# Kernel optimization log

Measured on AMD Instinct MI355X. Metric: run time of the kernel, lower is better.

Reference implementation:

```python
import jax, jax.numpy as jnp
import numpy as np

# dims
B, V, IMG = 16, 2, 224
G, PATCH, SG = 7, 14, 16
D, NH, L = 768, 12, 12
DH = D // NH            # 64
P = DH // 4             # rope frequencies per axis (2D axial RoPE)
N = G * G               # 49 glimpse tokens
S = SG * SG             # 256 scene tokens
GSIZE = G * PATCH       # 98 px glimpse


def _ln(x, w, b):
    m = x.mean(-1, keepdims=True)
    v = ((x - m) ** 2).mean(-1, keepdims=True)
    return (x - m) * jax.lax.rsqrt(v + 1e-6) * w + b


def _rope(pos, periods):
    # pos [B,N,2] -> cos,sin [B,N,2P]  (x freqs then y freqs)
    ang = (pos[..., :, None] / periods).reshape(pos.shape[0], pos.shape[1], -1)
    return jnp.cos(ang), jnp.sin(ang)


def _apply_rope(x, cos, sin):
    # x [B,H,N,DH]; cos/sin [B,N,DH//2]
    c = cos[:, None, :, :]
    s = sin[:, None, :, :]
    xr = x.reshape(x.shape[0], x.shape[1], x.shape[2], DH // 2, 2)
    x1, x2 = xr[..., 0], xr[..., 1]
    return jnp.stack([x1 * c - x2 * s, x1 * s + x2 * c], -1).reshape(x.shape)


def _heads(x):
    return x.reshape(x.shape[0], x.shape[1], NH, DH).transpose(0, 2, 1, 3)


def _merge(x):
    return x.transpose(0, 2, 1, 3).reshape(x.shape[0], x.shape[2], D)


def _attn(q, k, v):
    a = jax.nn.softmax(jnp.einsum('bhqd,bhkd->bhqk', q, k) / jnp.sqrt(jnp.float32(DH)), axis=-1)
    return jnp.einsum('bhqk,bhkd->bhqd', a, v)


def _cross(xq, xkv, qw, qb, kvw, kvb, ow, ob, rq, rkv):
    q = _heads(xq @ qw.T + qb)
    kv = xkv @ kvw.T + kvb
    k, v = _heads(kv[..., :D]), _heads(kv[..., D:])
    q = _apply_rope(q, *rq)
    k = _apply_rope(k, *rkv)
    return _merge(_attn(q, k, v)) @ ow.T + ob


def _bilinear(img, py, px):
    # img [C,H,W], py/px [GSIZE] pixel coords -> [C,GSIZE,GSIZE]
    Hh, Ww = img.shape[1], img.shape[2]
    y0 = jnp.clip(jnp.floor(py), 0, Hh - 2).astype(jnp.int32)
    x0 = jnp.clip(jnp.floor(px), 0, Ww - 2).astype(jnp.int32)
    wy = jnp.clip(py - y0, 0.0, 1.0)[None, :, None]
    wx = jnp.clip(px - x0, 0.0, 1.0)[None, None, :]
    g0, g1 = img[:, y0, :], img[:, y0 + 1, :]
    v00, v01 = g0[:, :, x0], g0[:, :, x0 + 1]
    v10, v11 = g1[:, :, x0], g1[:, :, x0 + 1]
    return (v00 * (1 - wy) + v10 * wy) * (1 - wx) + (v01 * (1 - wy) + v11 * wy) * wx


def _extract(images, c, s):
    # crop a [-1,1]-normalized glimpse of half-width `scale` at `center`
    lin = jnp.linspace(-1.0, 1.0, GSIZE)
    gy = c[:, 1:2] + s[:, None] * lin
    gx = c[:, 0:1] + s[:, None] * lin
    py = (gy + 1.0) * 0.5 * (images.shape[2] - 1)
    px = (gx + 1.0) * 0.5 * (images.shape[3] - 1)
    return jax.vmap(_bilinear)(images, py, px)


def _forward(images, centers, scales, patch_w, patch_b, scene_tokens,
             ln1_w, ln1_b, ln2_w, ln2_b, qkv_w, qkv_b, attn_out_w, attn_out_b,
             mlp_w1, mlp_b1, mlp_w2, mlp_b2,
             read_q_w, read_q_b, read_kv_w, read_kv_b, read_out_w, read_out_b, read_gate,
             write_q_w, write_q_b, write_kv_w, write_kv_b, write_out_w, write_out_b, write_gate):
    periods = 100.0 ** (jnp.arange(P, dtype=jnp.float32) / P)
    lin_s = jnp.linspace(-1.0, 1.0, SG)
    ys, xs = jnp.meshgrid(lin_s, lin_s, indexing='ij')
    scene_pos = jnp.broadcast_to(jnp.stack([xs.ravel(), ys.ravel()], -1), (B, S, 2))
    scene_rope = _rope(scene_pos, periods)
    lin_g = jnp.linspace(-1.0, 1.0, G)
    yg, xg = jnp.meshgrid(lin_g, lin_g, indexing='ij')
    goffs = jnp.stack([xg.ravel(), yg.ravel()], -1)  # [N,2]

    scene = jnp.broadcast_to(scene_tokens, (B, S, D))
    for vp in range(V):
        glimpse = _extract(images, centers[vp], scales[vp])  # [B,3,98,98]
        t = jax.lax.conv_general_dilated(glimpse, patch_w, (PATCH, PATCH), 'VALID',
                                         dimension_numbers=('NCHW', 'OIHW', 'NCHW'))
        local = t.reshape(B, D, N).transpose(0, 2, 1) + patch_b  # [B,49,D]
        lpos = centers[vp][:, None, :] + scales[vp][:, None, None] * goffs
        lrope = _rope(lpos, periods)
        for i in range(L):
            local = local + read_gate[i] * _cross(local, scene,
                read_q_w[i], read_q_b[i], read_kv_w[i], read_kv_b[i],
                read_out_w[i], read_out_b[i], lrope, scene_rope)
            # ViT block with RoPE self-attention
            h = _ln(local, ln1_w[i], ln1_b[i])
            qkv = h @ qkv_w[i].T + qkv_b[i]
            q, k, v = _heads(qkv[..., :D]), _heads(qkv[..., D:2 * D]), _heads(qkv[..., 2 * D:])
            q = _apply_rope(q, *lrope)
            k = _apply_rope(k, *lrope)
            local = local + _merge(_attn(q, k, v)) @ attn_out_w[i].T + attn_out_b[i]
            h = _ln(local, ln2_w[i], ln2_b[i])
            local = local + jax.nn.gelu(h @ mlp_w1[i].T + mlp_b1[i]) @ mlp_w2[i].T + mlp_b2[i]
            scene = scene + write_gate[i] * _cross(scene, local,
                write_q_w[i], write_q_b[i], write_kv_w[i], write_kv_b[i],
                write_out_w[i], write_out_b[i], scene_rope, lrope)
    return scene  # [B,S,D]


def setup_inputs() -> dict:
    key = jax.random.key(0)
    ks = iter(jax.random.split(key, 40))
    std = 0.02
    d = {}
    d['images'] = jax.random.normal(next(ks), (B, 3, IMG, IMG), jnp.float32)
    d['centers'] = jax.random.uniform(next(ks), (V, B, 2), jnp.float32, -0.5, 0.5)
    d['scales'] = jax.random.uniform(next(ks), (V, B), jnp.float32, 0.2, 0.4)
    d['patch_w'] = jax.random.normal(next(ks), (D, 3, PATCH, PATCH), jnp.float32) * std
    d['patch_b'] = jnp.zeros((D,), jnp.float32)
    d['scene_tokens'] = jax.random.normal(next(ks), (1, S, D), jnp.float32) / jnp.sqrt(jnp.float32(D))
    d['ln1_w'] = jnp.ones((L, D), jnp.float32); d['ln1_b'] = jnp.zeros((L, D), jnp.float32)
    d['ln2_w'] = jnp.ones((L, D), jnp.float32); d['ln2_b'] = jnp.zeros((L, D), jnp.float32)
    d['qkv_w'] = jax.random.normal(next(ks), (L, 3 * D, D), jnp.float32) * std
    d['qkv_b'] = jnp.zeros((L, 3 * D), jnp.float32)
    d['attn_out_w'] = jax.random.normal(next(ks), (L, D, D), jnp.float32) * std
    d['attn_out_b'] = jnp.zeros((L, D), jnp.float32)
    d['mlp_w1'] = jax.random.normal(next(ks), (L, 4 * D, D), jnp.float32) * std
    d['mlp_b1'] = jnp.zeros((L, 4 * D), jnp.float32)
    d['mlp_w2'] = jax.random.normal(next(ks), (L, D, 4 * D), jnp.float32) * std
    d['mlp_b2'] = jnp.zeros((L, D), jnp.float32)
    for pre in ('read', 'write'):
        d[pre + '_q_w'] = jax.random.normal(next(ks), (L, D, D), jnp.float32) * std
        d[pre + '_q_b'] = jnp.zeros((L, D), jnp.float32)
        d[pre + '_kv_w'] = jax.random.normal(next(ks), (L, 2 * D, D), jnp.float32) * std
        d[pre + '_kv_b'] = jnp.zeros((L, 2 * D), jnp.float32)
        d[pre + '_out_w'] = jax.random.normal(next(ks), (L, D, D), jnp.float32) * std
        d[pre + '_out_b'] = jnp.zeros((L, D), jnp.float32)
        d[pre + '_gate'] = jax.random.normal(next(ks), (L, D), jnp.float32) * 0.1
    return d


def reference(images, centers, scales, patch_w, patch_b, scene_tokens,
              ln1_w, ln1_b, ln2_w, ln2_b, qkv_w, qkv_b, attn_out_w, attn_out_b,
              mlp_w1, mlp_b1, mlp_w2, mlp_b2,
              read_q_w, read_q_b, read_kv_w, read_kv_b, read_out_w, read_out_b, read_gate,
              write_q_w, write_q_b, write_kv_w, write_kv_b, write_out_w, write_out_b, write_gate):
    return _forward(images, centers, scales, patch_w, patch_b, scene_tokens,
                    ln1_w, ln1_b, ln2_w, ln2_b, qkv_w, qkv_b, attn_out_w, attn_out_b,
                    mlp_w1, mlp_b1, mlp_w2, mlp_b2,
                    read_q_w, read_q_b, read_kv_w, read_kv_b, read_out_w, read_out_b, read_gate,
                    write_q_w, write_q_b, write_kv_w, write_kv_b, write_out_w, write_out_b, write_gate)
```

## Files before the change

### kernel.cpp

```cpp
#include <hip/hip_runtime.h>

#define B_ 16
#define V_ 2
#define D_ 768
#define NH_ 12
#define L_ 12
#define DH_ 64
#define N_ 49
#define S_ 256

__device__ __forceinline__ unsigned short f2bf(float f) {
  unsigned int u = __builtin_bit_cast(unsigned int, f);
  u += 0x7fffu + ((u >> 16) & 1u);
  return (unsigned short)(u >> 16);
}
__device__ __forceinline__ float bf2f(unsigned short h) {
  unsigned int u = ((unsigned int)h) << 16;
  return __builtin_bit_cast(float, u);
}
__device__ __forceinline__ float bflo(unsigned int w) {
  return __builtin_bit_cast(float, w << 16);
}
__device__ __forceinline__ float bfhi(unsigned int w) {
  return __builtin_bit_cast(float, w & 0xffff0000u);
}
__device__ __forceinline__ unsigned int packbf2(float a, float b) {
  return (unsigned int)f2bf(a) | ((unsigned int)f2bf(b) << 16);
}

using bf16x8 = __attribute__((ext_vector_type(8))) __bf16;
using u16x8  = __attribute__((ext_vector_type(8))) unsigned short;
using f32x4  = __attribute__((ext_vector_type(4))) float;

__device__ __forceinline__ void g2l16(const unsigned short* g, unsigned short* l) {
  __builtin_amdgcn_global_load_lds(
      (const __attribute__((address_space(1))) unsigned int*)g,
      (__attribute__((address_space(3))) unsigned int*)l, 16, 0, 0);
}

template <int BM, int BN, int BK, bool SWZ>
__global__ __launch_bounds__(256) void gemm_v6(
    const unsigned short* __restrict__ A, int lda,
    const unsigned short* __restrict__ W, int ldw,
    const float* __restrict__ bias,
    float* __restrict__ Cf, unsigned short* __restrict__ Cb, int ldc,
    const float* __restrict__ res, const float* __restrict__ gate,
    int M, int N, int K, int epi)
{
  __shared__ unsigned short As[2][BM * BK];
  __shared__ unsigned short Bs[2][BN * BK];
  constexpr int FM = BM / 32, FN = BN / 32;
  constexpr int CPR = BK / 8;
  constexpr int LPS = (BM + BN) * BK / 2048;
  int m0, n0;
  if (SWZ) {
    const int gx = gridDim.x;
    const int nwg = gx * gridDim.y;
    const int orig = blockIdx.y * gx + blockIdx.x;
    const int xcd = orig & 7, rem = orig >> 3;
    const int qq = nwg >> 3, rr = nwg & 7;
    const int wgid = (xcd < rr ? xcd * (qq + 1) : rr * (qq + 1) + (xcd - rr) * qq) + rem;
    m0 = (wgid % gx) * BM; n0 = (wgid / gx) * BN;
  } else {
    m0 = blockIdx.x * BM; n0 = blockIdx.y * BN;
  }
  const int tid = threadIdx.x, lane = tid & 63, wid = tid >> 6;
  const int wr = wid >> 1, wc = wid & 1;
  const int fr = lane & 15, kq8 = lane >> 4;

  f32x4 acc[FM][FN];
#pragma unroll
  for (int mi = 0; mi < FM; ++mi)
#pragma unroll
    for (int ni = 0; ni < FN; ++ni) acc[mi][ni] = f32x4{0.f, 0.f, 0.f, 0.f};

  auto stage = [&](int buf, int k0) {
    const unsigned short* Ab = A + (size_t)m0 * lda + k0;
    const unsigned short* Bb = W + (size_t)n0 * ldw + k0;
#pragma unroll
    for (int ra = 0; ra < BM * BK / 2048; ++ra) {
      int c = ra * 256 + tid;
      int row = c / CPR, slot = c % CPR;
      int gslot = slot ^ (row & 7);
      g2l16(Ab + (size_t)row * lda + gslot * 8, &As[buf][c * 8]);
    }
#pragma unroll
    for (int rb = 0; rb < BN * BK / 2048; ++rb) {
      int c = rb * 256 + tid;
      int row = c / CPR, slot = c % CPR;
      int gslot = slot ^ (row & 7);
      g2l16(Bb + (size_t)row * ldw + gslot * 8, &Bs[buf][c * 8]);
    }
  };

  const int nt = K / BK;
  stage(0, 0);
  int cur = 0;
  for (int t = 0; t < nt; ++t) {
    if (t + 1 < nt) {
      stage(cur ^ 1, (t + 1) * BK);
      asm volatile("s_waitcnt vmcnt(%0)" :: "i"(LPS) : "memory");
    } else {
      asm volatile("s_waitcnt vmcnt(0)" ::: "memory");
    }
    __builtin_amdgcn_s_barrier();
#pragma unroll
    for (int ks = 0; ks < BK / 32; ++ks) {
      bf16x8 av[FM], bv[FN];
#pragma unroll
      for (int mi = 0; mi < FM; ++mi) {
        int row = wr * (BM / 2) + mi * 16 + fr;
        int idx = row * BK + (((ks * 4 + kq8) ^ (row & 7)) << 3);
        av[mi] = __builtin_bit_cast(bf16x8, *(const u16x8*)&As[cur][idx]);
      }
#pragma unroll
      for (int ni = 0; ni < FN; ++ni) {
        int row = wc * (BN / 2) + ni * 16 + fr;
        int idx = row * BK + (((ks * 4 + kq8) ^ (row & 7)) << 3);
        bv[ni] = __builtin_bit_cast(bf16x8, *(const u16x8*)&Bs[cur][idx]);
      }
#pragma unroll
      for (int mi = 0; mi < FM; ++mi)
#pragma unroll
        for (int ni = 0; ni < FN; ++ni)
          acc[mi][ni] = __builtin_amdgcn_mfma_f32_16x16x32_bf16(av[mi], bv[ni], acc[mi][ni], 0, 0, 0);
    }
    __builtin_amdgcn_s_barrier();
    cur ^= 1;
  }

  const int er = (lane >> 4) * 4, ec = lane & 15;
#pragma unroll
  for (int mi = 0; mi < FM; ++mi)
#pragma unroll
    for (int ni = 0; ni < FN; ++ni) {
      int gc = n0 + wc * (BN / 2) + ni * 16 + ec;
      float bi = bias ? bias[gc] : 0.0f;
      float gg = gate ? gate[gc] : 1.0f;
#pragma unroll
      for (int i = 0; i < 4; ++i) {
        int gr = m0 + wr * (BM / 2) + mi * 16 + er + i;
        if (gr < M) {
          float v = acc[mi][ni][i] + bi;
          if (epi == 1) {
            v = v / (1.0f + __expf(-1.59576912f * (v + 0.044715f * v * v * v)));
          } else if (epi == 2) {
            v = res[(size_t)gr * ldc + gc] + gg * v;
          }
          if (Cf) Cf[(size_t)gr * ldc + gc] = v;
          if (Cb) Cb[(size_t)gr * ldc + gc] = f2bf(v);
        }
      }
    }
}

template <int LKPAD>
__global__ __launch_bounds__(256) void attn_mfma(
    const unsigned short* __restrict__ Q, int ldq, int qoff, int Lq,
    const unsigned short* __restrict__ KV, int ldkv, int koff, int voff, int Lk,
    const float* __restrict__ cq, const float* __restrict__ sq, int rbq,
    const float* __restrict__ ck, const float* __restrict__ sk, int rbk,
    unsigned short* __restrict__ Out)
{
  constexpr int NT = LKPAD / 16;
  constexpr int NKS = LKPAD / 32;
  __shared__ unsigned short Kb[LKPAD * 64];
  __shared__ unsigned short Vt[64 * LKPAD];
  __shared__ unsigned short Qs[4][16 * 64];
  __shared__ unsigned short Pl[4][16 * LKPAD];
  const int b = blockIdx.x / NH_, h = blockIdx.x - b * NH_;
  const int tid = threadIdx.x, lane = tid & 63, wid = tid >> 6;

  for (int idx = tid; idx < LKPAD * 32; idx += 256) {
    int t = idx >> 5, m = idx & 31;
    int d = 2 * m;
    int ksl = (t << 6) + (((m >> 2) ^ (t & 7)) << 3) + ((m & 3) << 1);
    int vs0 = d * LKPAD + (((t >> 3) ^ (d & 7)) << 3) + (t & 7);
    int vs1 = (d + 1) * LKPAD + (((t >> 3) ^ ((d + 1) & 7)) << 3) + (t & 7);
    if (t < Lk) {
      size_t rowb = ((size_t)b * Lk + t) * ldkv;
      unsigned int kw = *(const unsigned int*)(KV + rowb + koff + h * DH_ + d);
      unsigned int vw = *(const unsigned int*)(KV + rowb + voff + h * DH_ + d);
      float k1 = bflo(kw), k2 = bfhi(kw);
      size_t ri = (size_t)b * rbk + (size_t)t * 32 + m;
      float c = ck[ri], s = sk[ri];
      *(unsigned int*)&Kb[ksl] = packbf2((k1 * c - k2 * s) * 0.125f, (k1 * s + k2 * c) * 0.125f);
      Vt[vs0] = (unsigned short)(vw & 0xffff);
      Vt[vs1] = (unsigned short)(vw >> 16);
    } else {
      *(unsigned int*)&Kb[ksl] = 0;
      Vt[vs0] = 0; Vt[vs1] = 0;
    }
  }
  const int qbase = blockIdx.y * 64 + wid * 16;
  for (int idx = lane; idx < 16 * 32; idx += 64) {
    int r = idx >> 5, m = idx & 31;
    int gq = qbase + r;
    unsigned int qr = 0;
    if (gq < Lq) {
      unsigned int qw = *(const unsigned int*)(Q + ((size_t)b * Lq + gq) * ldq + qoff + h * DH_ + 2 * m);
      float q1 = bflo(qw), q2 = bfhi(qw);
      size_t ri = (size_t)b * rbq + (size_t)gq * 32 + m;
      float c = cq[ri], s = sq[ri];
      qr = packbf2(q1 * c - q2 * s, q1 * s + q2 * c);
    }
    *(unsigned int*)&Qs[wid][(r << 6) + (((m >> 2) ^ (r & 7)) << 3) + ((m & 3) << 1)] = qr;
  }
  __syncthreads();

  const int fr = lane & 15, g = lane >> 4;
  bf16x8 qa[2];
#pragma unroll
  for (int ks = 0; ks < 2; ++ks)
    qa[ks] = __builtin_bit_cast(bf16x8,
        *(const u16x8*)&Qs[wid][(fr << 6) + ((((ks << 2) + g) ^ (fr & 7)) << 3)]);

  f32x4 sv[NT];
  __builtin_amdgcn_s_setprio(1);
#pragma unroll
  for (int t = 0; t < NT; ++t) {
    int key = (t << 4) + fr;
    f32x4 a = {0.f, 0.f, 0.f, 0.f};
#pragma unroll
    for (int ks = 0; ks < 2; ++ks) {
      bf16x8 kb = __builtin_bit_cast(bf16x8,
          *(const u16x8*)&Kb[(key << 6) + ((((ks << 2) + g) ^ (key & 7)) << 3)]);
      a = __builtin_amdgcn_mfma_f32_16x16x32_bf16(qa[ks], kb, a, 0, 0, 0);
    }
    sv[t] = a;
  }
  __builtin_amdgcn_s_setprio(0);
#pragma unroll
  for (int t = 0; t < NT; ++t) {
    int key = (t << 4) + fr;
    if (key >= Lk) sv[t] = f32x4{-1e30f, -1e30f, -1e30f, -1e30f};
  }
  f32x4 mx = sv[0];
#pragma unroll
  for (int t = 1; t < NT; ++t)
#pragma unroll
    for (int i = 0; i < 4; ++i) mx[i] = fmaxf(mx[i], sv[t][i]);
#pragma unroll
  for (int off = 1; off <= 8; off <<= 1)
#pragma unroll
    for (int i = 0; i < 4; ++i) mx[i] = fmaxf(mx[i], __shfl_xor(mx[i], off));
  f32x4 sm = {0.f, 0.f, 0.f, 0.f};
#pragma unroll
  for (int t = 0; t < NT; ++t)
#pragma unroll
    for (int i = 0; i < 4; ++i) {
      float e = __expf(sv[t][i] - mx[i]);
      sv[t][i] = e;
      sm[i] += e;
    }
#pragma unroll
  for (int off = 1; off <= 8; off <<= 1)
#pragma unroll
    for (int i = 0; i < 4; ++i) sm[i] += __shfl_xor(sm[i], off);
  f32x4 inv;
#pragma unroll
  for (int i = 0; i < 4; ++i) inv[i] = 1.0f / sm[i];
#pragma unroll
  for (int t = 0; t < NT; ++t) {
    int key = (t << 4) + fr;
    int chunk = key >> 3;
#pragma unroll
    for (int i = 0; i < 4; ++i) {
      int row = (g << 2) + i;
      Pl[wid][row * LKPAD + ((chunk ^ (row & 7)) << 3) + (key & 7)] = f2bf(sv[t][i]);
// ... 117 lines not shown
  float xx = -1.0f + 2.0f * j / 15.0f;
  float yy = -1.0f + 2.0f * i / 15.0f;
  float coord = (m < 16) ? xx : yy;
  float per = powf(100.0f, (float)(m & 15) / 16.0f);
  float ang = coord / per;
  c[idx] = cosf(ang); s[idx] = sinf(ang);
}

__global__ void rope_local_k(float* __restrict__ c, float* __restrict__ s,
                             const float* __restrict__ ctr, const float* __restrict__ scl) {
  int idx = blockIdx.x * 256 + threadIdx.x;
  if (idx >= B_ * N_ * 32) return;
  int b = idx / (N_ * 32);
  int r = idx - b * (N_ * 32);
  int pch = r >> 5, m = r & 31;
  int py = pch / 7, px = pch - py * 7;
  float cx = ctr[b * 2], cy = ctr[b * 2 + 1], sc = scl[b];
  float gx = cx + sc * ((px - 3.0f) / 3.0f);
  float gy = cy + sc * ((py - 3.0f) / 3.0f);
  float coord = (m < 16) ? gx : gy;
  float per = powf(100.0f, (float)(m & 15) / 16.0f);
  float ang = coord / per;
  c[idx] = cosf(ang); s[idx] = sinf(ang);
}

__global__ void im2col_k(unsigned short* __restrict__ xb, const float* __restrict__ img,
                         const float* __restrict__ ctr, const float* __restrict__ scl) {
  int idx = blockIdx.x * 256 + threadIdx.x;
  if (idx >= 784 * 768) return;
  int row = idx / 768, col = idx - row * 768;
  float val = 0.0f;
  if (col < 588) {
    int b = row / 49, pch = row - b * 49;
    int c = col / 196, rr = col - c * 196;
    int i = rr / 14, j = rr - i * 14;
    int py = pch / 7, px = pch - py * 7;
    int gyi = py * 14 + i, gxi = px * 14 + j;
    float cx = ctr[b * 2], cy = ctr[b * 2 + 1], sc = scl[b];
    float gy = cy + sc * (-1.0f + 2.0f * gyi / 97.0f);
    float gx = cx + sc * (-1.0f + 2.0f * gxi / 97.0f);
    float pyi = (gy + 1.0f) * 0.5f * 223.0f;
    float pxi = (gx + 1.0f) * 0.5f * 223.0f;
    float y0f = fminf(fmaxf(floorf(pyi), 0.0f), 222.0f);
    float x0f = fminf(fmaxf(floorf(pxi), 0.0f), 222.0f);
    int y0 = (int)y0f, x0 = (int)x0f;
    float wy = fminf(fmaxf(pyi - y0f, 0.0f), 1.0f);
    float wx = fminf(fmaxf(pxi - x0f, 0.0f), 1.0f);
    const float* base = img + (size_t)(b * 3 + c) * 224 * 224;
    float v00 = base[y0 * 224 + x0],       v01 = base[y0 * 224 + x0 + 1];
    float v10 = base[(y0 + 1) * 224 + x0], v11 = base[(y0 + 1) * 224 + x0 + 1];
    val = (v00 * (1.0f - wy) + v10 * wy) * (1.0f - wx) + (v01 * (1.0f - wy) + v11 * wy) * wx;
  }
  xb[idx] = f2bf(val);
}

extern "C" void kernel_launch(void* const* d_in, const int* in_sizes, int n_in,
                              void* d_out, int out_size, void* d_ws, size_t ws_size,
                              hipStream_t stream) {
  const float* images    = (const float*)d_in[0];
  const float* centers   = (const float*)d_in[1];
  const float* scales    = (const float*)d_in[2];
  const float* patch_w   = (const float*)d_in[3];
  const float* patch_b   = (const float*)d_in[4];
  const float* scene_tok = (const float*)d_in[5];
  const float* ln1_w = (const float*)d_in[6];
  const float* ln1_b = (const float*)d_in[7];
  const float* ln2_w = (const float*)d_in[8];
  const float* ln2_b = (const float*)d_in[9];
  const float* qkv_w = (const float*)d_in[10];
  const float* qkv_b = (const float*)d_in[11];
  const float* ao_w  = (const float*)d_in[12];
  const float* ao_b  = (const float*)d_in[13];
  const float* m1_w  = (const float*)d_in[14];
  const float* m1_b  = (const float*)d_in[15];
  const float* m2_w  = (const float*)d_in[16];
  const float* m2_b  = (const float*)d_in[17];
  const float* rq_w  = (const float*)d_in[18];
  const float* rq_b  = (const float*)d_in[19];
  const float* rkv_w = (const float*)d_in[20];
  const float* rkv_b = (const float*)d_in[21];
  const float* ro_w  = (const float*)d_in[22];
  const float* ro_b  = (const float*)d_in[23];
  const float* rgate = (const float*)d_in[24];
  const float* wq_w  = (const float*)d_in[25];
  const float* wq_b  = (const float*)d_in[26];
  const float* wkv_w = (const float*)d_in[27];
  const float* wkv_b = (const float*)d_in[28];
  const float* wo_w  = (const float*)d_in[29];
  const float* wo_b  = (const float*)d_in[30];
  const float* wgate = (const float*)d_in[31];

  float* scene_f = (float*)d_out;

  char* p = (char*)d_ws;
  auto alloc = [&](size_t bytes) { char* r = p; p += (bytes + 255) & ~(size_t)255; return (void*)r; };
  unsigned short* scene_bf = (unsigned short*)alloc((size_t)4096 * 768 * 2);
  float*          local_f  = (float*)alloc((size_t)784 * 768 * 4);
  unsigned short* local_bf = (unsigned short*)alloc((size_t)896 * 768 * 2);
  unsigned short* q_r_bf   = (unsigned short*)alloc((size_t)896 * 768 * 2);
  unsigned short* qrkv_bf  = (unsigned short*)alloc((size_t)4096 * 2304 * 2);
  unsigned short* kv_bf    = (unsigned short*)alloc((size_t)896 * 2304 * 2);
  unsigned short* kvq_bf   = (unsigned short*)alloc((size_t)896 * 2304 * 2);
  unsigned short* ln_bf    = (unsigned short*)alloc((size_t)896 * 768 * 2);
  unsigned short* act_bf   = (unsigned short*)alloc((size_t)4096 * 768 * 2);
  unsigned short* x_bf     = (unsigned short*)alloc((size_t)896 * 768 * 2);
  float* sc_cos = (float*)alloc((size_t)S_ * 32 * 4);
  float* sc_sin = (float*)alloc((size_t)S_ * 32 * 4);
  float* l_cos  = (float*)alloc((size_t)B_ * N_ * 32 * 4);
  float* l_sin  = (float*)alloc((size_t)B_ * N_ * 32 * 4);
  unsigned short* patch_wbf = (unsigned short*)alloc((size_t)768 * 768 * 2);
  float*          fb        = (float*)alloc((size_t)L_ * 2304 * 4);
  float*          fb2       = (float*)alloc((size_t)L_ * 2304 * 4);

  static const size_t REGSZ[9] = {589824, 1769472, 589824, 1769472, 589824,
                                  2359296, 2359296, 1769472, 589824};
  struct SegDef { const float* src; int reg; unsigned off; unsigned lsrc; int nl; };
  const SegDef SEGS[11] = {
    {rq_w,            0, 0,       589824,  L_},
    {wq_w,            1, 0,       589824,  L_},
    {rkv_w,           1, 589824,  1179648, L_},
    {ro_w,            2, 0,       589824,  L_},
    {qkv_w,           3, 0,       1769472, L_},
    {ao_w,            4, 0,       589824,  L_},
    {m1_w,            5, 0,       2359296, L_},
    {m2_w,            6, 0,       2359296, L_},
    {wkv_w,           7, 0,       1179648, L_},
    {rq_w + 589824,   7, 1179648, 589824,  L_ - 1},
    {wo_w,            8, 0,       589824,  L_},
  };
  size_t regBase[9];
  size_t perLayer = 0;
  {
    size_t cur = 0;
    for (int i = 0; i < 9; ++i) { regBase[i] = cur; cur += REGSZ[i] * L_; perLayer += REGSZ[i]; }
  }
  const size_t allElems = perLayer * L_;
  size_t usedBytes = (size_t)(p - (char*)d_ws);
  bool preconv = ws_size >= usedBytes + allElems * 2 + 4096;
  unsigned short* wbf = (unsigned short*)alloc((preconv ? allElems : perLayer) * 2);

  auto GQ = [&](const unsigned short* A, int lda, const unsigned short* Wp,
                const float* bias, float* Cf, unsigned short* Cb, int ldc,
                const float* res, const float* gt, int N, int epi) {
    gemm_v6<128, 128, 64, true><<<dim3(32, N / 128), 256, 0, stream>>>(
        A, lda, Wp, 768, bias, Cf, Cb, ldc, res, gt, 4096, N, 768, epi);
  };
  auto GW = [&](const unsigned short* A, int lda, const unsigned short* Wp,
                const float* bias, float* Cf, unsigned short* Cb, int ldc,
                const float* res, const float* gt, int N, int epi) {
    gemm_v6<128, 64, 64, true><<<dim3(32, N / 64), 256, 0, stream>>>(
        A, lda, Wp, 768, bias, Cf, Cb, ldc, res, gt, 4096, N, 768, epi);
  };
  auto GS = [&](const unsigned short* A, int lda, const unsigned short* Wp, int ldw,
                const float* bias, float* Cf, unsigned short* Cb, int ldc,
                const float* res, const float* gt, int N, int K, int epi) {
    gemm_v6<64, 64, 128, true><<<dim3(13, N / 64), 256, 0, stream>>>(
        A, lda, Wp, ldw, bias, Cf, Cb, ldc, res, gt, 784, N, K, epi);
  };

  {
    int total = B_ * S_ * D_;
    init_scene_k<<<(total + 255) / 256, 256, 0, stream>>>(scene_tok, scene_f, scene_bf, total);
    rope_scene_k<<<(S_ * 32 + 255) / 256, 256, 0, stream>>>(sc_cos, sc_sin);
    cvt_patch_k<<<(768 * 768 + 255) / 256, 256, 0, stream>>>(patch_w, patch_wbf);
    fbias_k<<<(L_ * 2304 + 255) / 256, 256, 0, stream>>>(wq_b, rkv_b, fb);
    fbias2_k<<<(L_ * 2304 + 255) / 256, 256, 0, stream>>>(wkv_b, rq_b, fb2);
    if (preconv) {
      CvtA cv;
      int blk = 0;
      for (int i = 0; i < 11; ++i) {
        cv.s[i] = SEGS[i].src;
        cv.d[i] = wbf + regBase[SEGS[i].reg] + SEGS[i].off;
        cv.lsrc[i] = SEGS[i].lsrc;
        cv.lstride[i] = (unsigned)REGSZ[SEGS[i].reg];
        blk += (int)((size_t)SEGS[i].lsrc * SEGS[i].nl / 2048);
        cv.blkEnd[i] = blk;
      }
      cvt_multi_k<<<blk, 256, 0, stream>>>(cv);
    }
  }

  for (int vp = 0; vp < V_; ++vp) {
    const float* ctr = centers + (size_t)vp * B_ * 2;
    const float* scl = scales + (size_t)vp * B_;
    rope_local_k<<<(B_ * N_ * 32 + 255) / 256, 256, 0, stream>>>(l_cos, l_sin, ctr, scl);
    im2col_k<<<(784 * 768 + 255) / 256, 256, 0, stream>>>(x_bf, images, ctr, scl);
    GS(x_bf, 768, patch_wbf, 768, patch_b, local_f, local_bf, 768,
       nullptr, nullptr, 768, 768, 0);

    for (int l = 0; l < L_; ++l) {
      const unsigned short* wR[9];
      if (preconv) {
        for (int rg = 0; rg < 9; ++rg)
          wR[rg] = wbf + regBase[rg] + (size_t)l * REGSZ[rg];
      } else {
        CvtA cv;
        int blk = 0;
        size_t cur = 0;
        size_t rb[9];
        for (int rg = 0; rg < 9; ++rg) { rb[rg] = cur; cur += REGSZ[rg]; wR[rg] = wbf + rb[rg]; }
        for (int i = 0; i < 11; ++i) {
          size_t srcl = (i == 9) ? (size_t)((l + 1) % L_) : (size_t)l;
          cv.s[i] = (i == 9 ? rq_w : SEGS[i].src) + srcl * SEGS[i].lsrc;
          cv.d[i] = wbf + rb[SEGS[i].reg] + SEGS[i].off;
          cv.lsrc[i] = SEGS[i].lsrc;
          cv.lstride[i] = (unsigned)REGSZ[SEGS[i].reg];
          blk += (int)(SEGS[i].lsrc / 2048);
          cv.blkEnd[i] = blk;
        }
        cvt_multi_k<<<blk, 256, 0, stream>>>(cv);
      }

      GQ(scene_bf, 768, wR[1], fb + (size_t)l * 2304,
         nullptr, qrkv_bf, 2304, nullptr, nullptr, 2304, 0);
      if (l == 0)
        GS(local_bf, 768, wR[0], 768, rq_b + l * 768,
           nullptr, q_r_bf, 768, nullptr, nullptr, 768, 768, 0);
      if (l == 0)
        attn_mfma<256><<<dim3(B_ * NH_, 1), 256, 0, stream>>>(q_r_bf, 768, 0, 49,
            qrkv_bf, 2304, 768, 1536, 256, l_cos, l_sin, N_ * 32, sc_cos, sc_sin, 0, act_bf);
      else
        attn_mfma<256><<<dim3(B_ * NH_, 1), 256, 0, stream>>>(kvq_bf, 2304, 1536, 49,
            qrkv_bf, 2304, 768, 1536, 256, l_cos, l_sin, N_ * 32, sc_cos, sc_sin, 0, act_bf);
      GS(act_bf, 768, wR[2], 768, ro_b + l * 768,
         local_f, local_bf, 768, local_f, rgate + l * 768, 768, 768, 2);
      ln_kernel<<<784, 256, 0, stream>>>(local_f, ln1_w + l * 768, ln1_b + l * 768, ln_bf);
      GS(ln_bf, 768, wR[3], 768, qkv_b + (size_t)l * 2304,
         nullptr, kv_bf, 2304, nullptr, nullptr, 2304, 768, 0);
      attn_mfma<64><<<dim3(B_ * NH_, 1), 256, 0, stream>>>(kv_bf, 2304, 0, 49,
          kv_bf, 2304, 768, 1536, 49, l_cos, l_sin, N_ * 32, l_cos, l_sin, N_ * 32, act_bf);
      GS(act_bf, 768, wR[4], 768, ao_b + l * 768,
         local_f, local_bf, 768, local_f, nullptr, 768, 768, 2);
      ln_kernel<<<784, 256, 0, stream>>>(local_f, ln2_w + l * 768, ln2_b + l * 768, ln_bf);
      GS(ln_bf, 768, wR[5], 768, m1_b + (size_t)l * 3072,
         nullptr, act_bf, 3072, nullptr, nullptr, 3072, 768, 1);
      GS(act_bf, 3072, wR[6], 3072, m2_b + l * 768,
         local_f, local_bf, 768, local_f, nullptr, 768, 3072, 2);
      GS(local_bf, 768, wR[7], 768, fb2 + (size_t)l * 2304,
         nullptr, kvq_bf, 2304, nullptr, nullptr, 2304, 768, 0);
      attn_mfma<64><<<dim3(B_ * NH_, 4), 256, 0, stream>>>(qrkv_bf, 2304, 0, 256,
          kvq_bf, 2304, 0, 768, 49, sc_cos, sc_sin, 0, l_cos, l_sin, N_ * 32, act_bf);
      GW(act_bf, 768, wR[8], wo_b + l * 768,
         scene_f, scene_bf, 768, scene_f, wgate + l * 768, 768, 2);
    }
  }
}
```

Baseline: 6.240 ms.

## Fuse whole forward into persistent megakernel with software grid barriers

Replaces the hundreds of per-layer kernel launches with a single persistent kernel of 256 blocks × 512 threads that runs every phase (im2col, GEMMs, attention, layernorm) in sequence, separated by an atomic-counter grid barrier. The aim is to remove launch overhead and the tail idle time between small kernels. The cost is fixed tile sizes and occupancy (one large block per CU with 144KB shared memory), per-phase work loops that may balance poorly on the small 784-row GEMMs, and the risk of deadlock if not all 256 blocks are co-resident.

```diff
diff --git a/kernel.cpp b/kernel.cpp
--- a/kernel.cpp
+++ b/kernel.cpp
@@ -67,13 +67,11 @@
   const int tid = threadIdx.x, lane = tid & 63, wid = tid >> 6;
   const int wr = wid >> 1, wc = wid & 1;
   const int fr = lane & 15, kq8 = lane >> 4;
-
   f32x4 acc[FM][FN];
 #pragma unroll
   for (int mi = 0; mi < FM; ++mi)
 #pragma unroll
     for (int ni = 0; ni < FN; ++ni) acc[mi][ni] = f32x4{0.f, 0.f, 0.f, 0.f};
-
   auto stage = [&](int buf, int k0) {
     const unsigned short* Ab = A + (size_t)m0 * lda + k0;
     const unsigned short* Bb = W + (size_t)n0 * ldw + k0;
@@ -81,18 +79,15 @@
     for (int ra = 0; ra < BM * BK / 2048; ++ra) {
       int c = ra * 256 + tid;
       int row = c / CPR, slot = c % CPR;
-      int gslot = slot ^ (row & 7);
-      g2l16(Ab + (size_t)row * lda + gslot * 8, &As[buf][c * 8]);
+      g2l16(Ab + (size_t)row * lda + (slot ^ (row & 7)) * 8, &As[buf][c * 8]);
     }
 #pragma unroll
     for (int rb = 0; rb < BN * BK / 2048; ++rb) {
       int c = rb * 256 + tid;
       int row = c / CPR, slot = c % CPR;
-      int gslot = slot ^ (row & 7);
-      g2l16(Bb + (size_t)row * ldw + gslot * 8, &Bs[buf][c * 8]);
+      g2l16(Bb + (size_t)row * ldw + (slot ^ (row & 7)) * 8, &Bs[buf][c * 8]);
     }
   };
-
   const int nt = K / BK;
   stage(0, 0);
   int cur = 0;
@@ -128,7 +123,6 @@
     __builtin_amdgcn_s_barrier();
     cur ^= 1;
   }
-
   const int er = (lane >> 4) * 4, ec = lane & 15;
 #pragma unroll
   for (int mi = 0; mi < FM; ++mi)
@@ -170,7 +164,6 @@
   __shared__ unsigned short Pl[4][16 * LKPAD];
   const int b = blockIdx.x / NH_, h = blockIdx.x - b * NH_;
   const int tid = threadIdx.x, lane = tid & 63, wid = tid >> 6;
-
   for (int idx = tid; idx < LKPAD * 32; idx += 256) {
     int t = idx >> 5, m = idx & 31;
     int d = 2 * m;
@@ -207,14 +200,12 @@
     *(unsigned int*)&Qs[wid][(r << 6) + (((m >> 2) ^ (r & 7)) << 3) + ((m & 3) << 1)] = qr;
   }
   __syncthreads();
-
   const int fr = lane & 15, g = lane >> 4;
   bf16x8 qa[2];
 #pragma unroll
   for (int ks = 0; ks < 2; ++ks)
     qa[ks] = __builtin_bit_cast(bf16x8,
         *(const u16x8*)&Qs[wid][(fr << 6) + ((((ks << 2) + g) ^ (fr & 7)) << 3)]);
-
   f32x4 sv[NT];
   __builtin_amdgcn_s_setprio(1);
 #pragma unroll
@@ -438,6 +429,425 @@
     val = (v00 * (1.0f - wy) + v10 * wy) * (1.0f - wx) + (v01 * (1.0f - wy) + v11 * wy) * wx;
   }
   xb[idx] = f2bf(val);
+}
+
+struct MegaP {
+  const float *centers, *scales, *images;
+  const float *patch_b, *rq_b, *ro_b, *qkv_b, *ao_b, *m1_b, *m2_b, *wo_b;
+  const float *ln1_w, *ln1_b, *ln2_w, *ln2_b;
+  const float *rgate, *wgate, *fb, *fb2;
+  const unsigned short *patch_wbf, *wbf;
+  float *scene_f, *local_f;
+  unsigned short *scene_bf, *local_bf, *q_r_bf, *qrkv_bf, *kv_bf, *kvq_bf, *ln_bf, *act_bf, *x_bf;
+  float *sc_cos, *sc_sin, *l_cos, *l_sin;
+  unsigned int *bar;
+};
+
+__device__ __forceinline__ void gridbar(unsigned int* bar) {
+  __syncthreads();
+  if (threadIdx.x == 0) {
+    __threadfence();
+    unsigned int g = __hip_atomic_load(&bar[1], __ATOMIC_RELAXED, __HIP_MEMORY_SCOPE_AGENT);
+    unsigned int a = __hip_atomic_fetch_add(&bar[0], 1u, __ATOMIC_ACQ_REL, __HIP_MEMORY_SCOPE_AGENT);
+    if (a == 255u) {
+      __hip_atomic_store(&bar[0], 0u, __ATOMIC_RELAXED, __HIP_MEMORY_SCOPE_AGENT);
+      __hip_atomic_fetch_add(&bar[1], 1u, __ATOMIC_RELEASE, __HIP_MEMORY_SCOPE_AGENT);
+    } else {
+      while (__hip_atomic_load(&bar[1], __ATOMIC_ACQUIRE, __HIP_MEMORY_SCOPE_AGENT) == g)
+        __builtin_amdgcn_s_sleep(2);
+    }
+    __threadfence();
+  }
+  __syncthreads();
+}
+
+template <int BM, int BN, int BK>
+__device__ void gemm_ph(char* smemc,
+    const unsigned short* __restrict__ A, int lda,
+    const unsigned short* __restrict__ W, int ldw,
+    const float* __restrict__ bias,
+    float* __restrict__ Cf, unsigned short* __restrict__ Cb, int ldc,
+    const float* __restrict__ res, const float* __restrict__ gate,
+    int M, int N, int K, int epi)
+{
+  unsigned short* As = (unsigned short*)smemc;
+  unsigned short* Bs = As + 2 * BM * BK;
+  constexpr int RS = BM / 4, CS = BN / 2;
+  constexpr int FM = RS / 16, FN = CS / 16;
+  constexpr int CPR = BK / 8;
+  constexpr int LPS = (BM + BN) * BK / 4096;
+  const int tid = threadIdx.x, lane = tid & 63, wid = tid >> 6;
+  const int wr = wid >> 1, wc = wid & 1;
+  const int fr = lane & 15, kq8 = lane >> 4;
+  const int nmb = (M + BM - 1) / BM, nnb = N / BN;
+
+  for (int vb = blockIdx.x; vb < nmb * nnb; vb += gridDim.x) {
+    const int m0 = (vb % nmb) * BM, n0 = (vb / nmb) * BN;
+    f32x4 acc[FM][FN];
+#pragma unroll
+    for (int mi = 0; mi < FM; ++mi)
+#pragma unroll
+      for (int ni = 0; ni < FN; ++ni) acc[mi][ni] = f32x4{0.f, 0.f, 0.f, 0.f};
+    auto stage = [&](int buf, int k0) {
+      const unsigned short* Ab = A + (size_t)m0 * lda + k0;
+      const unsigned short* Bb = W + (size_t)n0 * ldw + k0;
+#pragma unroll
+      for (int ra = 0; ra < BM * BK / 4096; ++ra) {
+        int c = ra * 512 + tid;
+        int row = c / CPR, slot = c % CPR;
+        g2l16(Ab + (size_t)row * lda + (slot ^ (row & 7)) * 8, As + buf * BM * BK + c * 8);
+      }
+#pragma unroll
+      for (int rb = 0; rb < BN * BK / 4096; ++rb) {
+        int c = rb * 512 + tid;
+        int row = c / CPR, slot = c % CPR;
+        g2l16(Bb + (size_t)row * ldw + (slot ^ (row & 7)) * 8, Bs + buf * BN * BK + c * 8);
+      }
+    };
+    const int nt = K / BK;
+    stage(0, 0);
+    int cur = 0;
+    for (int t = 0; t < nt; ++t) {
+      if (t + 1 < nt) {
+        stage(cur ^ 1, (t + 1) * BK);
+        asm volatile("s_waitcnt vmcnt(%0)" :: "i"(LPS) : "memory");
+      } else {
+        asm volatile("s_waitcnt vmcnt(0)" ::: "memory");
+      }
+      __builtin_amdgcn_s_barrier();
+#pragma unroll
+      for (int ks = 0; ks < BK / 32; ++ks) {
+        bf16x8 av[FM], bv[FN];
+#pragma unroll
+        for (int mi = 0; mi < FM; ++mi) {
+          int row = wr * RS + mi * 16 + fr;
+          int idx = row * BK + (((ks * 4 + kq8) ^ (row & 7)) << 3);
+          av[mi] = __builtin_bit_cast(bf16x8, *(const u16x8*)&As[cur * BM * BK + idx]);
+        }
+#pragma unroll
+        for (int ni = 0; ni < FN; ++ni) {
+          int row = wc * CS + ni * 16 + fr;
+          int idx = row * BK + (((ks * 4 + kq8) ^ (row & 7)) << 3);
+          bv[ni] = __builtin_bit_cast(bf16x8, *(const u16x8*)&Bs[cur * BN * BK + idx]);
+        }
+#pragma unroll
+        for (int mi = 0; mi < FM; ++mi)
+#pragma unroll
+          for (int ni = 0; ni < FN; ++ni)
+            acc[mi][ni] = __builtin_amdgcn_mfma_f32_16x16x32_bf16(av[mi], bv[ni], acc[mi][ni], 0, 0, 0);
+      }
+      __builtin_amdgcn_s_barrier();
+      cur ^= 1;
+    }
+    const int er = (lane >> 4) * 4, ec = lane & 15;
+#pragma unroll
+    for (int mi = 0; mi < FM; ++mi)
+#pragma unroll
+      for (int ni = 0; ni < FN; ++ni) {
+        int gc = n0 + wc * CS + ni * 16 + ec;
+        float bi = bias ? bias[gc] : 0.0f;
+        float gg = gate ? gate[gc] : 1.0f;
+#pragma unroll
+        for (int i = 0; i < 4; ++i) {
+          int gr = m0 + wr * RS + mi * 16 + er + i;
+          if (gr < M) {
+            float v = acc[mi][ni][i] + bi;
+            if (epi == 1) {
+              v = v / (1.0f + __expf(-1.59576912f * (v + 0.044715f * v * v * v)));
+            } else if (epi == 2) {
+              v = res[(size_t)gr * ldc + gc] + gg * v;
+            }
+            if (Cf) Cf[(size_t)gr * ldc + gc] = v;
+            if (Cb) Cb[(size_t)gr * ldc + gc] = f2bf(v);
+          }
+        }
+      }
+    __builtin_amdgcn_s_barrier();
+  }
+}
+
+template <int LKPAD>
+__device__ void attn_ph(char* smemc,
+    const unsigned short* __restrict__ Q, int ldq, int qoff, int Lq,
+    const unsigned short* __restrict__ KV, int ldkv, int koff, int voff, int Lk,
+    const float* __restrict__ cq, const float* __restrict__ sq, int rbq,
+    const float* __restrict__ ck, const float* __restrict__ sk, int rbk,
+    unsigned short* __restrict__ Out, int nspl)
+{
+  constexpr int NT = LKPAD / 16;
+  constexpr int NKS = LKPAD / 32;
+  unsigned short* Kb = (unsigned short*)smemc;
+  unsigned short* Vt = Kb + LKPAD * 64;
+  unsigned short* Qs = Vt + 64 * LKPAD;
+  unsigned short* Pl = Qs + 8 * 1024;
+  const int tid = threadIdx.x, lane = tid & 63, wid = tid >> 6;
+  const int fr = lane & 15, g = lane >> 4;
+  const int nvb = B_ * NH_ * nspl;
+  for (int vb = blockIdx.x; vb < nvb; vb += gridDim.x) {
+    const int yb = vb % nspl, bh = vb / nspl;
+    const int b = bh / NH_, h = bh - b * NH_;
+    for (int idx = tid; idx < LKPAD * 32; idx += 512) {
+      int t = idx >> 5, m = idx & 31;
+      int d = 2 * m;
+      int ksl = (t << 6) + (((m >> 2) ^ (t & 7)) << 3) + ((m & 3) << 1);
+      int vs0 = d * LKPAD + (((t >> 3) ^ (d & 7)) << 3) + (t & 7);
+      int vs1 = (d + 1) * LKPAD + (((t >> 3) ^ ((d + 1) & 7)) << 3) + (t & 7);
+      if (t < Lk) {
+        size_t rowb = ((size_t)b * Lk + t) * ldkv;
+        unsigned int kw = *(const unsigned int*)(KV + rowb + koff + h * DH_ + d);
+        unsigned int vw = *(const unsigned int*)(KV + rowb + voff + h * DH_ + d);
+        float k1 = bflo(kw), k2 = bfhi(kw);
+        size_t ri = (size_t)b * rbk + (size_t)t * 32 + m;
+        float c = ck[ri], s = sk[ri];
+        *(unsigned int*)&Kb[ksl] = packbf2((k1 * c - k2 * s) * 0.125f, (k1 * s + k2 * c) * 0.125f);
+        Vt[vs0] = (unsigned short)(vw & 0xffff);
+        Vt[vs1] = (unsigned short)(vw >> 16);
+      } else {
+        *(unsigned int*)&Kb[ksl] = 0;
+        Vt[vs0] = 0; Vt[vs1] = 0;
+      }
+    }
+    const int qbase = yb * 128 + wid * 16;
+    unsigned short* Qw = Qs + wid * 1024;
+    unsigned short* Pw = Pl + wid * 16 * LKPAD;
+    for (int idx = lane; idx < 16 * 32; idx += 64) {
+      int r = idx >> 5, m = idx & 31;
+      int gq = qbase + r;
+      unsigned int qr = 0;
+      if (gq < Lq) {
+        unsigned int qw = *(const unsigned int*)(Q + ((size_t)b * Lq + gq) * ldq + qoff + h * DH_ + 2 * m);
+        float q1 = bflo(qw), q2 = bfhi(qw);
+        size_t ri = (size_t)b * rbq + (size_t)gq * 32 + m;
+        float c = cq[ri], s = sq[ri];
+        qr = packbf2(q1 * c - q2 * s, q1 * s + q2 * c);
+      }
+      *(unsigned int*)&Qw[(r << 6) + (((m >> 2) ^ (r & 7)) << 3) + ((m & 3) << 1)] = qr;
+    }
+    __syncthreads();
+    if (qbase < Lq) {
+      bf16x8 qa[2];
+#pragma unroll
+      for (int ks = 0; ks < 2; ++ks)
+        qa[ks] = __builtin_bit_cast(bf16x8,
+            *(const u16x8*)&Qw[(fr << 6) + ((((ks << 2) + g) ^ (fr & 7)) << 3)]);
+      f32x4 sv[NT];
+      __builtin_amdgcn_s_setprio(1);
+#pragma unroll
+      for (int t = 0; t < NT; ++t) {
+        int key = (t << 4) + fr;
+        f32x4 a = {0.f, 0.f, 0.f, 0.f};
+#pragma unroll
+        for (int ks = 0; ks < 2; ++ks) {
+          bf16x8 kb = __builtin_bit_cast(bf16x8,
+              *(const u16x8*)&Kb[(key << 6) + ((((ks << 2) + g) ^ (key & 7)) << 3)]);
+          a = __builtin_amdgcn_mfma_f32_16x16x32_bf16(qa[ks], kb, a, 0, 0, 0);
+        }
+        sv[t] = a;
+      }
+      __builtin_amdgcn_s_setprio(0);
+#pragma unroll
+      for (int t = 0; t < NT; ++t) {
+        int key = (t << 4) + fr;
+        if (key >= Lk) sv[t] = f32x4{-1e30f, -1e30f, -1e30f, -1e30f};
+      }
+      f32x4 mx = sv[0];
+#pragma unroll
+      for (int t = 1; t < NT; ++t)
+#pragma unroll
+        for (int i = 0; i < 4; ++i) mx[i] = fmaxf(mx[i], sv[t][i]);
+#pragma unroll
+      for (int off = 1; off <= 8; off <<= 1)
+#pragma unroll
+        for (int i = 0; i < 4; ++i) mx[i] = fmaxf(mx[i], __shfl_xor(mx[i], off));
+      f32x4 sm = {0.f, 0.f, 0.f, 0.f};
+#pragma unroll
+      for (int t = 0; t < NT; ++t)
+#pragma unroll
+        for (int i = 0; i < 4; ++i) {
+          float e = __expf(sv[t][i] - mx[i]);
+          sv[t][i] = e;
+          sm[i] += e;
+        }
+#pragma unroll
+      for (int off = 1; off <= 8; off <<= 1)
+#pragma unroll
+        for (int i = 0; i < 4; ++i) sm[i] += __shfl_xor(sm[i], off);
+      f32x4 inv;
+#pragma unroll
+      for (int i = 0; i < 4; ++i) inv[i] = 1.0f / sm[i];
+#pragma unroll
+      for (int t = 0; t < NT; ++t) {
+        int key = (t << 4) + fr;
+        int chunk = key >> 3;
+#pragma unroll
+        for (int i = 0; i < 4; ++i) {
+          int row = (g << 2) + i;
+          Pw[row * LKPAD + ((chunk ^ (row & 7)) << 3) + (key & 7)] = f2bf(sv[t][i]);
+        }
+      }
+      f32x4 oacc[4];
+#pragma unroll
+      for (int n = 0; n < 4; ++n) oacc[n] = f32x4{0.f, 0.f, 0.f, 0.f};
+      __builtin_amdgcn_s_setprio(1);
+#pragma unroll
+      for (int ks = 0; ks < NKS; ++ks) {
+        int chunk = (ks << 2) + g;
+        bf16x8 pa = __builtin_bit_cast(bf16x8,
+            *(const u16x8*)&Pw[fr * LKPAD + ((chunk ^ (fr & 7)) << 3)]);
+#pragma unroll
+        for (int n = 0; n < 4; ++n) {
+          int drow = (n << 4) + fr;
+          bf16x8 vbv = __builtin_bit_cast(bf16x8,
+              *(const u16x8*)&Vt[drow * LKPAD + ((chunk ^ (drow & 7)) << 3)]);
+          oacc[n] = __builtin_amdgcn_mfma_f32_16x16x32_bf16(pa, vbv, oacc[n], 0, 0, 0);
+        }
+      }
+      __builtin_amdgcn_s_setprio(0);
+#pragma unroll
+      for (int n = 0; n < 4; ++n)
+#pragma unroll
+        for (int i = 0; i < 4; ++i) {
+          int gq = qbase + (g << 2) + i;
+          if (gq < Lq)
+            Out[((size_t)b * Lq + gq) * D_ + h * DH_ + (n << 4) + fr] = f2bf(oacc[n][i] * inv[i]);
+        }
+    }
+    __syncthreads();
+  }
+}
+
+__device__ void ln_ph(const float* __restrict__ X, const float* __restrict__ w,
+                      const float* __restrict__ bsh, unsigned short* __restrict__ Out) {
+  const int lane = threadIdx.x & 63, wid = threadIdx.x >> 6;
+  for (int row = blockIdx.x * 8 + wid; row < 784; row += gridDim.x * 8) {
+    const float* x = X + (size_t)row * 768;
+    float v[12];
+    float s = 0.f;
+#pragma unroll
+    for (int j = 0; j < 12; ++j) { v[j] = x[lane + 64 * j]; s += v[j]; }
+    for (int o = 32; o; o >>= 1) s += __shfl_xor(s, o);
+    float mean = s * (1.0f / 768.0f);
+    float q = 0.f;
+#pragma unroll
+    for (int j = 0; j < 12; ++j) { float d = v[j] - mean; q += d * d; }
+    for (int o = 32; o; o >>= 1) q += __shfl_xor(q, o);
+    float rstd = rsqrtf(q * (1.0f / 768.0f) + 1e-6f);
+#pragma unroll
+    for (int j = 0; j < 12; ++j)
+      Out[(size_t)row * 768 + lane + 64 * j] =
+          f2bf((v[j] - mean) * rstd * w[lane + 64 * j] + bsh[lane + 64 * j]);
+  }
+}
+
+__device__ void view_pre_ph(const MegaP& P, int vp) {
+  const float* ctr = P.centers + vp * B_ * 2;
+  const float* scl = P.scales + vp * B_;
+  for (int idx = blockIdx.x * 512 + threadIdx.x; idx < 784 * 768; idx += 256 * 512) {
+    int row = idx / 768, col = idx - row * 768;
+    float val = 0.0f;
+    if (col < 588) {
+      int b = row / 49, pch = row - b * 49;
+      int c = col / 196, rr = col - c * 196;
+      int i = rr / 14, j = rr - i * 14;
+      int py = pch / 7, px = pch - py * 7;
+      int gyi = py * 14 + i, gxi = px * 14 + j;
+      float cx = ctr[b * 2], cy = ctr[b * 2 + 1], sc = scl[b];
+      float gy = cy + sc * (-1.0f + 2.0f * gyi / 97.0f);
+      float gx = cx + sc * (-1.0f + 2.0f * gxi / 97.0f);
+      float pyi = (gy + 1.0f) * 0.5f * 223.0f;
+      float pxi = (gx + 1.0f) * 0.5f * 223.0f;
+      float y0f = fminf(fmaxf(floorf(pyi), 0.0f), 222.0f);
+      float x0f = fminf(fmaxf(floorf(pxi), 0.0f), 222.0f);
+      int y0 = (int)y0f, x0 = (int)x0f;
+      float wy = fminf(fmaxf(pyi - y0f, 0.0f), 1.0f);
+      float wx = fminf(fmaxf(pxi - x0f, 0.0f), 1.0f);
+      const float* base = P.images + (size_t)(b * 3 + c) * 224 * 224;
+      float v00 = base[y0 * 224 + x0],       v01 = base[y0 * 224 + x0 + 1];
+      float v10 = base[(y0 + 1) * 224 + x0], v11 = base[(y0 + 1) * 224 + x0 + 1];
+      val = (v00 * (1.0f - wy) + v10 * wy) * (1.0f - wx) + (v01 * (1.0f - wy) + v11 * wy) * wx;
+    }
+    P.x_bf[idx] = f2bf(val);
+    if (idx < B_ * N_ * 32) {
+      int b = idx / (N_ * 32);
+      int r = idx - b * (N_ * 32);
+      int pch = r >> 5, m = r & 31;
+      int py = pch / 7, px = pch - py * 7;
+      float cx = ctr[b * 2], cy = ctr[b * 2 + 1], sc = scl[b];
+      float gx = cx + sc * ((px - 3.0f) / 3.0f);
+      float gy = cy + sc * ((py - 3.0f) / 3.0f);
+      float coord = (m < 16) ? gx : gy;
+      float per = powf(100.0f, (float)(m & 15) / 16.0f);
+      float ang = coord / per;
+      P.l_cos[idx] = cosf(ang); P.l_sin[idx] = sinf(ang);
+    }
+  }
+}
+
+__constant__ size_t c_REGSZ[9] = {589824, 1769472, 589824, 1769472, 589824,
+                                  2359296, 2359296, 1769472, 589824};
+
+__global__ __launch_bounds__(512) void mega_k(MegaP P) {
+  __shared__ char smem[147456];
+  size_t regBase[9];
+  {
+    size_t cur = 0;
+    for (int i = 0; i < 9; ++i) { regBase[i] = cur; cur += c_REGSZ[i] * L_; }
+  }
+  for (int vp = 0; vp < V_; ++vp) {
+    view_pre_ph(P, vp); gridbar(P.bar);
+    gemm_ph<64, 64, 128>(smem, P.x_bf, 768, P.patch_wbf, 768, P.patch_b,
+                         P.local_f, P.local_bf, 768, nullptr, nullptr, 784, 768, 768, 0);
+    gridbar(P.bar);
+    for (int l = 0; l < L_; ++l) {
+      const unsigned short* wR[9];
+      for (int rg = 0; rg < 9; ++rg) wR[rg] = P.wbf + regBase[rg] + (size_t)l * c_REGSZ[rg];
+      gemm_ph<128, 128, 64>(smem, P.scene_bf, 768, wR[1], 768, P.fb + (size_t)l * 2304,
+                            nullptr, P.qrkv_bf, 2304, nullptr, nullptr, 4096, 2304, 768, 0);
+      gridbar(P.bar);
+      if (l == 0) {
+        gemm_ph<64, 64, 128>(smem, P.local_bf, 768, wR[0], 768, P.rq_b + l * 768,
+                             nullptr, P.q_r_bf, 768, nullptr, nullptr, 784, 768, 768, 0);
+        gridbar(P.bar);
+        attn_ph<256>(smem, P.q_r_bf, 768, 0, 49, P.qrkv_bf, 2304, 768, 1536, 256,
+                     P.l_cos, P.l_sin, N_ * 32, P.sc_cos, P.sc_sin, 0, P.act_bf, 1);
+      } else {
+        attn_ph<256>(smem, P.kvq_bf, 2304, 1536, 49, P.qrkv_bf, 2304, 768, 1536, 256,
+                     P.l_cos, P.l_sin, N_ * 32, P.sc_cos, P.sc_sin, 0, P.act_bf, 1);
+      }
+      gridbar(P.bar);
+      gemm_ph<64, 64, 128>(smem, P.act_bf, 768, wR[2], 768, P.ro_b + l * 768,
+                           P.local_f, P.local_bf, 768, P.local_f, P.rgate + l * 768, 784, 768, 768, 2);
+      gridbar(P.bar);
+      ln_ph(P.local_f, P.ln1_w + l * 768, P.ln1_b + l * 768, P.ln_bf);
+      gridbar(P.bar);
+      gemm_ph<64, 64, 128>(smem, P.ln_bf, 768, wR[3], 768, P.qkv_b + (size_t)l * 2304,
+                           nullptr, P.kv_bf, 2304, nullptr, nullptr, 784, 2304, 768, 0);
+      gridbar(P.bar);
+      attn_ph<64>(smem, P.kv_bf, 2304, 0, 49, P.kv_bf, 2304, 768, 1536, 49,
+                  P.l_cos, P.l_sin, N_ * 32, P.l_cos, P.l_sin, N_ * 32, P.act_bf, 1);
+      gridbar(P.bar);
+      gemm_ph<64, 64, 128>(smem, P.act_bf, 768, wR[4], 768, P.ao_b + l * 768,
+                           P.local_f, P.local_bf, 768, P.local_f, nullptr, 784, 768, 768, 2);
+      gridbar(P.bar);
+      ln_ph(P.local_f, P.ln2_w + l * 768, P.ln2_b + l * 768, P.ln_bf);
+      gridbar(P.bar);
+      gemm_ph<64, 64, 128>(smem, P.ln_bf, 768, wR[5], 768, P.m1_b + (size_t)l * 3072,
+                           nullptr, P.act_bf, 3072, nullptr, nullptr, 784, 3072, 768, 1);
+      gridbar(P.bar);
+      gemm_ph<64, 64, 128>(smem, P.act_bf, 3072, wR[6], 3072, P.m2_b + l * 768,
+                           P.local_f, P.local_bf, 768, P.local_f, nullptr, 784, 768, 3072, 2);
+      gridbar(P.bar);
+      gemm_ph<64, 64, 128>(smem, P.local_bf, 768, wR[7], 768, P.fb2 + (size_t)l * 2304,
+                           nullptr, P.kvq_bf, 2304, nullptr, nullptr, 784, 2304, 768, 0);
+      gridbar(P.bar);
+      attn_ph<64>(smem, P.qrkv_bf, 2304, 0, 256, P.kvq_bf, 2304, 0, 768, 49,
+                  P.sc_cos, P.sc_sin, 0, P.l_cos, P.l_sin, N_ * 32, P.act_bf, 2);
+      gridbar(P.bar);
+      gemm_ph<128, 64, 64>(smem, P.act_bf, 768, wR[8], 768, P.wo_b + l * 768,
+                           P.scene_f, P.scene_bf, 768, P.scene_f, P.wgate + l * 768, 4096, 768, 768, 2);
+      gridbar(P.bar);
+    }
+  }
 }
 
 extern "C" void kernel_launch(void* const* d_in, const int* in_sizes, int n_in,
@@ -497,6 +907,7 @@
   unsigned short* patch_wbf = (unsigned short*)alloc((size_t)768 * 768 * 2);
   float*          fb        = (float*)alloc((size_t)L_ * 2304 * 4);
   float*          fb2       = (float*)alloc((size_t)L_ * 2304 * 4);
+  unsigned int*   bar       = (unsigned int*)alloc(256);
 
   static const size_t REGSZ[9] = {589824, 1769472, 589824, 1769472, 589824,
                                   2359296, 2359296, 1769472, 589824};
@@ -525,6 +936,47 @@
   bool preconv = ws_size >= usedBytes + allElems * 2 + 4096;
   unsigned short* wbf = (unsigned short*)alloc((preconv ? allElems : perLayer) * 2);
 
+  {
+    int total = B_ * S_ * D_;
+    init_scene_k<<<(total + 255) / 256, 256, 0, stream>>>(scene_tok, scene_f, scene_bf, total);
+    rope_scene_k<<<(S_ * 32 + 255) / 256, 256, 0, stream>>>(sc_cos, sc_sin);
+    cvt_patch_k<<<(768 * 768 + 255) / 256, 256, 0, stream>>>(patch_w, patch_wbf);
+    fbias_k<<<(L_ * 2304 + 255) / 256, 256, 0, stream>>>(wq_b, rkv_b, fb);
+    fbias2_k<<<(L_ * 2304 + 255) / 256, 256, 0, stream>>>(wkv_b, rq_b, fb2);
+    if (preconv) {
+      CvtA cv;
+      int blk = 0;
+      for (int i = 0; i < 11; ++i) {
+        cv.s[i] = SEGS[i].src;
+        cv.d[i] = wbf + regBase[SEGS[i].reg] + SEGS[i].off;
+        cv.lsrc[i] = SEGS[i].lsrc;
+        cv.lstride[i] = (unsigned)REGSZ[SEGS[i].reg];
+        blk += (int)((size_t)SEGS[i].lsrc * SEGS[i].nl / 2048);
+        cv.blkEnd[i] = blk;
+      }
+      cvt_multi_k<<<blk, 256, 0, stream>>>(cv);
+    }
+  }
+
+  if (preconv) {
+    hipMemsetAsync(bar, 0, 8, stream);
+    MegaP mp;
+    mp.centers = centers; mp.scales = scales; mp.images = images;
+    mp.patch_b = patch_b; mp.rq_b = rq_b; mp.ro_b = ro_b; mp.qkv_b = qkv_b;
+    mp.ao_b = ao_b; mp.m1_b = m1_b; mp.m2_b = m2_b; mp.wo_b = wo_b;
+    mp.ln1_w = ln1_w; mp.ln1_b = ln1_b; mp.ln2_w = ln2_w; mp.ln2_b = ln2_b;
+    mp.rgate = rgate; mp.wgate = wgate; mp.fb = fb; mp.fb2 = fb2;
+    mp.patch_wbf = patch_wbf; mp.wbf = wbf;
+    mp.scene_f = scene_f; mp.local_f = local_f;
+    mp.scene_bf = scene_bf; mp.local_bf = local_bf; mp.q_r_bf = q_r_bf;
+    mp.qrkv_bf = qrkv_bf; mp.kv_bf = kv_bf; mp.kvq_bf = kvq_bf;
+    mp.ln_bf = ln_bf; mp.act_bf = act_bf; mp.x_bf = x_bf;
+    mp.sc_cos = sc_cos; mp.sc_sin = sc_sin; mp.l_cos = l_cos; mp.l_sin = l_sin;
+    mp.bar = bar;
+    mega_k<<<256, 512, 0, stream>>>(mp);
+    return;
+  }
+
   auto GQ = [&](const unsigned short* A, int lda, const unsigned short* Wp,
                 const float* bias, float* Cf, unsigned short* Cb, int ldc,
                 const float* res, const float* gt, int N, int epi) {
@@ -544,28 +996,6 @@
         A, lda, Wp, ldw, bias, Cf, Cb, ldc, res, gt, 784, N, K, epi);
   };
 
-  {
-    int total = B_ * S_ * D_;
-    init_scene_k<<<(total + 255) / 256, 256, 0, stream>>>(scene_tok, scene_f, scene_bf, total);
-    rope_scene_k<<<(S_ * 32 + 255) / 256, 256, 0, stream>>>(sc_cos, sc_sin);
-    cvt_patch_k<<<(768 * 768 + 255) / 256, 256, 0, stream>>>(patch_w, patch_wbf);
-    fbias_k<<<(L_ * 2304 + 255) / 256, 256, 0, stream>>>(wq_b, rkv_b, fb);
-    fbias2_k<<<(L_ * 2304 + 255) / 256, 256, 0, stream>>>(wkv_b, rq_b, fb2);
-    if (preconv) {
-      CvtA cv;
-      int blk = 0;
-      for (int i = 0; i < 11; ++i) {
-        cv.s[i] = SEGS[i].src;
-        cv.d[i] = wbf + regBase[SEGS[i].reg] + SEGS[i].off;
-        cv.lsrc[i] = SEGS[i].lsrc;
-        cv.lstride[i] = (unsigned)REGSZ[SEGS[i].reg];
-        blk += (int)((size_t)SEGS[i].lsrc * SEGS[i].nl / 2048);
-        cv.blkEnd[i] = blk;
-      }
-      cvt_multi_k<<<blk, 256, 0, stream>>>(cv);
-    }
-  }
-
   for (int vp = 0; vp < V_; ++vp) {
     const float* ctr = centers + (size_t)vp * B_ * 2;
     const float* scl = scales + (size_t)vp * B_;
@@ -573,29 +1003,23 @@
     im2col_k<<<(784 * 768 + 255) / 256, 256, 0, stream>>>(x_bf, images, ctr, scl);
     GS(x_bf, 768, patch_wbf, 768, patch_b, local_f, local_bf, 768,
        nullptr, nullptr, 768, 768, 0);
-
     for (int l = 0; l < L_; ++l) {
       const unsigned short* wR[9];
-      if (preconv) {
-        for (int rg = 0; rg < 9; ++rg)
-          wR[rg] = wbf + regBase[rg] + (size_t)l * REGSZ[rg];
-      } else {
-        CvtA cv;
-        int blk = 0;
-        size_t cur = 0;
-        size_t rb[9];
-        for (int rg = 0; rg < 9; ++rg) { rb[rg] = cur; cur += REGSZ[rg]; wR[rg] = wbf + rb[rg]; }
-        for (int i = 0; i < 11; ++i) {
-          size_t srcl = (i == 9) ? (size_t)((l + 1) % L_) : (size_t)l;
-          cv.s[i] = (i == 9 ? rq_w : SEGS[i].src) + srcl * SEGS[i].lsrc;
-          cv.d[i] = wbf + rb[SEGS[i].reg] + SEGS[i].off;
-          cv.lsrc[i] = SEGS[i].lsrc;
-          cv.lstride[i] = (unsigned)REGSZ[SEGS[i].reg];
-          blk += (int)(SEGS[i].lsrc / 2048);
-          cv.blkEnd[i] = blk;
-        }
-        cvt_multi_k<<<blk, 256, 0, stream>>>(cv);
-      }
+      CvtA cv;
+      int blk = 0;
+      size_t cur = 0;
+      size_t rb[9];
+      for (int rg = 0; rg < 9; ++rg) { rb[rg] = cur; cur += REGSZ[rg]; wR[rg] = wbf + rb[rg]; }
+      for (int i = 0; i < 11; ++i) {
+        size_t srcl = (i == 9) ? (size_t)((l + 1) % L_) : (size_t)l;
+        cv.s[i] = (i == 9 ? rq_w : SEGS[i].src) + srcl * SEGS[i].lsrc;
+        cv.d[i] = wbf + rb[SEGS[i].reg] + SEGS[i].off;
+        cv.lsrc[i] = SEGS[i].lsrc;
+        cv.lstride[i] = (unsigned)REGSZ[SEGS[i].reg];
+        blk += (int)(SEGS[i].lsrc / 2048);
+        cv.blkEnd[i] = blk;
+      }
+      cvt_multi_k<<<blk, 256, 0, stream>>>(cv);
 
       GQ(scene_bf, 768, wR[1], fb + (size_t)l * 2304,
          nullptr, qrkv_bf, 2304, nullptr, nullptr, 2304, 0);
```

Result: slower. 23.46 ms (+276.0%).
